# Kernel tuning notes

Measured on AMD Instinct MI355X. Metric: run time of the kernel, lower is better.

Reference implementation:

```python
import jax, jax.numpy as jnp
import numpy as np

BETA = 0.001  # commitment loss weight from __init__ default


def setup_inputs() -> dict:
    key = jax.random.key(0)
    k1, k2 = jax.random.split(key)
    N, INPUT_DIM = 8192, 1024
    S, K, D = 32, 1024, 32  # nsplits, num_embeddings, embedding_dim
    z = jax.random.normal(k1, (N, INPUT_DIM), dtype=jnp.float32)
    # Stacked codebook weights: one [K, D] embedding table per split.
    W = jax.random.normal(k2, (S, K, D), dtype=jnp.float32)
    return {"z": z, "W": W}


def reference(z, W):
    N, INPUT_DIM = z.shape
    S, K, D = W.shape
    zc = z.reshape(N, S, D)  # per-split chunks, matches torch.chunk(z, S, -1)
    # Squared euclidean distances ||z||^2 + ||w||^2 - 2 z.w  -> [N, S, K]
    d2 = (
        jnp.sum(zc * zc, axis=-1, keepdims=True)
        + jnp.sum(W * W, axis=-1)[None, :, :]
        - 2.0 * jnp.einsum("nsd,skd->nsk", zc, W)
    )
    idx = jnp.argmin(d2, axis=-1)  # [N, S]
    # Gather nearest codes: W[s, idx[n, s]] -> [N, S, D]
    zq = W[jnp.arange(S)[None, :], idx]
    # Sum over splits of per-split mse means; equal split sizes so this is
    # S * mean over the whole tensor.
    sg = jax.lax.stop_gradient
    loss = S * (
        jnp.mean((sg(zq) - zc) ** 2) + BETA * jnp.mean((zq - sg(zc)) ** 2)
    )
    # Straight-through estimator
    zq_st = zc + sg(zq - zc)
    return zq_st.reshape(N, INPUT_DIM), loss
```

## Files before the change

### kernel.cpp

```cpp
#include <hip/hip_runtime.h>
#include <math.h>

#define NN 8192
#define SS 32
#define DD 32
#define KK 1024
#define OUT_ELEMS ((size_t)NN * SS * DD)

#define LOSS_SCALE (32.0f * 1.001f / 8388608.0f)

typedef _Float16 half8 __attribute__((ext_vector_type(8)));
typedef float   floatx4 __attribute__((ext_vector_type(4)));

#define CH_TILES 4
#define CHUNK_K  (CH_TILES * 16)
#define NCHUNK   (KK / CHUNK_K)
#define RG 2
#define NBLOCKS ((NN / 128) * SS)


__global__ __launch_bounds__(256, 4) void vq_fused(const float* __restrict__ z,
                                                   const float* __restrict__ W,
                                                   float* __restrict__ out,
                                                   float* __restrict__ part) {
    __shared__ _Float16 bufH[2][CH_TILES][64][8];
    __shared__ _Float16 bufL[2][CH_TILES][64][8];
    __shared__ float    w2b[2][CHUNK_K];
    __shared__ int      lds_idx[4][32];
    __shared__ float    lds_part[4];

    const int s    = blockIdx.x & (SS - 1);
    const int n0b  = (blockIdx.x >> 5) * 128;
    const int tid  = threadIdx.x;
    const int wv   = tid >> 6;
    const int lane = tid & 63;
    const int col  = lane & 15;
    const int quad = lane >> 4;

    const float* __restrict__ Ws = W + (size_t)s * KK * DD;
    const int n0w = n0b + wv * 32;

    half8 zh[RG], zl[RG];
    #pragma unroll
    for (int rg = 0; rg < RG; ++rg) {
        const float* zp = z + (size_t)(n0w + rg * 16 + col) * (SS * DD) + s * DD + quad * 8;
        const float4 va = ((const float4*)zp)[0];
        const float4 vb = ((const float4*)zp)[1];
        const float src[8] = {va.x, va.y, va.z, va.w, vb.x, vb.y, vb.z, vb.w};
        #pragma unroll
        for (int j = 0; j < 8; ++j) {
            const float v = -2.0f * src[j];
            const _Float16 h = (_Float16)v;
            zh[rg][j] = h;
            zl[rg][j] = (_Float16)(v - (float)h);
        }
    }

    const float* __restrict__ stg = Ws + ((size_t)(wv * 16 + col)) * DD + quad * 8;

    floatx4 best[RG];
    int bi[RG][4];
    #pragma unroll
    for (int rg = 0; rg < RG; ++rg) {
        best[rg] = (floatx4){INFINITY, INFINITY, INFINITY, INFINITY};
        bi[rg][0] = bi[rg][1] = bi[rg][2] = bi[rg][3] = 0;
    }

    float4 pa = ((const float4*)stg)[0];
    float4 pb = ((const float4*)stg)[1];
    {
        const float src[8] = {pa.x, pa.y, pa.z, pa.w, pb.x, pb.y, pb.z, pb.w};
        half8 h8, l8; float ps = 0.0f;
        #pragma unroll
        for (int j = 0; j < 8; ++j) {
            const float v = src[j];
            ps = fmaf(v, v, ps);
            const _Float16 h = (_Float16)v;
            h8[j] = h;
            l8[j] = (_Float16)(v - (float)h);
        }
        ps += __shfl_xor(ps, 16, 64);
        ps += __shfl_xor(ps, 32, 64);
        *(half8*)&bufH[0][wv][lane][0] = h8;
        *(half8*)&bufL[0][wv][lane][0] = l8;
        if (quad == 0) w2b[0][wv * 16 + col] = ps;
    }
    __syncthreads();

    for (int c = 0; c < NCHUNK; ++c) {
        const int b = c & 1;
        if (c + 1 < NCHUNK) {
            const float* nsrc = stg + (size_t)(c + 1) * CHUNK_K * DD;
            pa = ((const float4*)nsrc)[0];
            pb = ((const float4*)nsrc)[1];
        }

        #pragma unroll
        for (int tt = 0; tt < CH_TILES; ++tt) {
            const half8 bh = *(const half8*)&bufH[b][tt][lane][0];
            const half8 bl = *(const half8*)&bufL[b][tt][lane][0];
            const float wv2 = w2b[b][tt * 16 + col];
            const floatx4 c0 = {wv2, wv2, wv2, wv2};
            const int tk = c * CH_TILES + tt;
            #pragma unroll
            for (int rg = 0; rg < RG; ++rg) {
                floatx4 acc = __builtin_amdgcn_mfma_f32_16x16x32_f16(zh[rg], bh, c0, 0, 0, 0);
                acc = __builtin_amdgcn_mfma_f32_16x16x32_f16(zl[rg], bh, acc, 0, 0, 0);
                acc = __builtin_amdgcn_mfma_f32_16x16x32_f16(zh[rg], bl, acc, 0, 0, 0);
                #pragma unroll
                for (int i = 0; i < 4; ++i) {
                    if (acc[i] < best[rg][i]) { best[rg][i] = acc[i]; bi[rg][i] = tk; }
                }
            }
        }

        if (c + 1 < NCHUNK) {
            const float src[8] = {pa.x, pa.y, pa.z, pa.w, pb.x, pb.y, pb.z, pb.w};
            half8 h8, l8; float ps = 0.0f;
            #pragma unroll
            for (int j = 0; j < 8; ++j) {
                const float v = src[j];
                ps = fmaf(v, v, ps);
                const _Float16 h = (_Float16)v;
                h8[j] = h;
                l8[j] = (_Float16)(v - (float)h);
            }
            ps += __shfl_xor(ps, 16, 64);
            ps += __shfl_xor(ps, 32, 64);
            const int nb = (c + 1) & 1;
            *(half8*)&bufH[nb][wv][lane][0] = h8;
            *(half8*)&bufL[nb][wv][lane][0] = l8;
            if (quad == 0) w2b[nb][wv * 16 + col] = ps;
            __syncthreads();
        }
    }

    #pragma unroll
    for (int rg = 0; rg < RG; ++rg) {
        #pragma unroll
        for (int i = 0; i < 4; ++i) {
            float v = best[rg][i];
            int   k = bi[rg][i] * 16 + col;
            #pragma unroll
            for (int m = 1; m < 16; m <<= 1) {
                const float vo = __shfl_xor(v, m, 64);
                const int   ko = __shfl_xor(k, m, 64);
                if (vo < v || (vo == v && ko < k)) { v = vo; k = ko; }
            }
            if (col == 0) lds_idx[wv][rg * 16 + quad * 4 + i] = k;
        }
    }
    __syncthreads();

    const int r  = lane & 31;
    const int dh = (lane >> 5) * 16;
    const int krow = lds_idx[wv][r];
    const float* wsrc = Ws + (size_t)krow * DD + dh;
    const size_t zoff = (size_t)(n0w + r) * (SS * DD) + s * DD + dh;
    const float* zsrc = z + zoff;
    float* od = out + zoff;
    float sq = 0.0f;
    #pragma unroll
    for (int cc = 0; cc < 4; ++cc) {
        const float4 wq = ((const float4*)wsrc)[cc];
        const float4 zv = ((const float4*)zsrc)[cc];
        const float d0 = wq.x - zv.x, d1 = wq.y - zv.y;
        const float d2 = wq.z - zv.z, d3 = wq.w - zv.w;
        sq = fmaf(d0, d0, sq); sq = fmaf(d1, d1, sq);
        sq = fmaf(d2, d2, sq); sq = fmaf(d3, d3, sq);
        ((float4*)od)[cc] = wq;
    }
    #pragma unroll
    for (int off = 32; off > 0; off >>= 1) sq += __shfl_down(sq, off, 64);

    if (lane == 0) lds_part[wv] = sq;
    __syncthreads();
    if (tid == 0)
        part[blockIdx.x] = lds_part[0] + lds_part[1] + lds_part[2] + lds_part[3];
}

__global__ __launch_bounds__(256) void vq_loss(const float* __restrict__ part,
                                               float* __restrict__ out) {
    __shared__ float l[4];
    const int tid = threadIdx.x;
    float sum = 0.0f;
    #pragma unroll
    for (int i = 0; i < NBLOCKS / 256; ++i) sum += part[tid + i * 256];
    #pragma unroll
    for (int off = 32; off > 0; off >>= 1) sum += __shfl_down(sum, off, 64);
    if ((tid & 63) == 0) l[tid >> 6] = sum;
    __syncthreads();
    if (tid == 0) out[OUT_ELEMS] = (l[0] + l[1] + l[2] + l[3]) * LOSS_SCALE;
}

extern "C" void kernel_launch(void* const* d_in, const int* in_sizes, int n_in,
                              void* d_out, int out_size, void* d_ws, size_t ws_size,
                              hipStream_t stream) {
    const float* z = (const float*)d_in[0];
    const float* W = (const float*)d_in[1];
    float* out  = (float*)d_out;
    float* part = (float*)d_ws;

    vq_fused<<<dim3(NBLOCKS), dim3(256), 0, stream>>>(z, W, out, part);
    vq_loss<<<dim3(1), dim3(256), 0, stream>>>(part, out);
}
```

Baseline: 152.5 us.

## Precompute split-fp16 codebook once in a prep kernel and stream fragments from global

Adds a prep kernel that converts W into hi/lo fp16 MFMA-ready fragments plus squared norms once per call. Before this, all 2048 blocks redid that conversion for their split. The main kernel now loads those fragments straight from global (L2) into registers with a two-tile register prefetch, and drops the LDS double buffer and its per-chunk __syncthreads. The cost is an extra kernel launch, extra workspace traffic, and more global-load latency that each wave must hide on its own.

```diff
diff --git a/kernel.cpp b/kernel.cpp
--- a/kernel.cpp
+++ b/kernel.cpp
@@ -12,22 +12,56 @@
 typedef _Float16 half8 __attribute__((ext_vector_type(8)));
 typedef float   floatx4 __attribute__((ext_vector_type(4)));
 
-#define CH_TILES 4
-#define CHUNK_K  (CH_TILES * 16)
-#define NCHUNK   (KK / CHUNK_K)
+#define TILES   (KK / 16)
 #define RG 2
 #define NBLOCKS ((NN / 128) * SS)
 
 
-__global__ __launch_bounds__(256, 4) void vq_fused(const float* __restrict__ z,
-                                                   const float* __restrict__ W,
-                                                   float* __restrict__ out,
-                                                   float* __restrict__ part) {
-    __shared__ _Float16 bufH[2][CH_TILES][64][8];
-    __shared__ _Float16 bufL[2][CH_TILES][64][8];
-    __shared__ float    w2b[2][CHUNK_K];
-    __shared__ int      lds_idx[4][32];
-    __shared__ float    lds_part[4];
+__global__ __launch_bounds__(256) void vq_prep(const float* __restrict__ W,
+                                               _Float16* __restrict__ wh,
+                                               _Float16* __restrict__ wl,
+                                               float* __restrict__ w2) {
+    const int g    = blockIdx.x * 256 + threadIdx.x;
+    const int l    = g & 63;
+    const int t    = (g >> 6) & 63;
+    const int s    = g >> 12;
+    const int col  = l & 15;
+    const int quad = l >> 4;
+    const int k    = t * 16 + col;
+
+    const float* src = W + ((size_t)s * KK + k) * DD + quad * 8;
+    const float4 a = ((const float4*)src)[0];
+    const float4 b = ((const float4*)src)[1];
+    const float v8[8] = {a.x, a.y, a.z, a.w, b.x, b.y, b.z, b.w};
+
+    float ps = 0.0f;
+    half8 h8, l8;
+    #pragma unroll
+    for (int j = 0; j < 8; ++j) {
+        const float v = v8[j];
+        ps = fmaf(v, v, ps);
+        const _Float16 h = (_Float16)v;
+        h8[j] = h;
+        l8[j] = (_Float16)(v - (float)h);
+    }
+    ps += __shfl_xor(ps, 16, 64);
+    ps += __shfl_xor(ps, 32, 64);
+    if (quad == 0) w2[(size_t)s * KK + k] = ps;
+
+    *(half8*)(wh + (size_t)g * 8) = h8;
+    *(half8*)(wl + (size_t)g * 8) = l8;
+}
+
+__global__ __launch_bounds__(256, 4) void vq_main(const float* __restrict__ z,
+                                                  const float* __restrict__ W,
+                                                  const _Float16* __restrict__ wh,
+                                                  const _Float16* __restrict__ wl,
+                                                  const float* __restrict__ w2,
+                                                  float* __restrict__ out,
+                                                  float* __restrict__ part) {
+    __shared__ float lds_w2[KK];
+    __shared__ int   lds_idx[4][32];
+    __shared__ float lds_part[4];
 
     const int s    = blockIdx.x & (SS - 1);
     const int n0b  = (blockIdx.x >> 5) * 128;
@@ -39,6 +73,11 @@
 
     const float* __restrict__ Ws = W + (size_t)s * KK * DD;
     const int n0w = n0b + wv * 32;
+
+    const float* w2s = w2 + (size_t)s * KK;
+    #pragma unroll
+    for (int j = 0; j < 4; ++j) lds_w2[tid + j * 256] = w2s[tid + j * 256];
+    __syncthreads();
 
     half8 zh[RG], zl[RG];
     #pragma unroll
@@ -56,7 +95,8 @@
         }
     }
 
-    const float* __restrict__ stg = Ws + ((size_t)(wv * 16 + col)) * DD + quad * 8;
+    const _Float16* __restrict__ bhp = wh + (size_t)s * (TILES * 64 * 8) + (size_t)lane * 8;
+    const _Float16* __restrict__ blp = wl + (size_t)s * (TILES * 64 * 8) + (size_t)lane * 8;
 
     floatx4 best[RG];
     int bi[RG][4];
@@ -66,42 +106,28 @@
         bi[rg][0] = bi[rg][1] = bi[rg][2] = bi[rg][3] = 0;
     }
 
-    float4 pa = ((const float4*)stg)[0];
-    float4 pb = ((const float4*)stg)[1];
-    {
-        const float src[8] = {pa.x, pa.y, pa.z, pa.w, pb.x, pb.y, pb.z, pb.w};
-        half8 h8, l8; float ps = 0.0f;
+    half8 bhA = *(const half8*)(bhp);
+    half8 blA = *(const half8*)(blp);
+    half8 bhB = *(const half8*)(bhp + 512);
+    half8 blB = *(const half8*)(blp + 512);
+
+    for (int t2 = 0; t2 < TILES / 2; ++t2) {
+        half8 nhA, nlA, nhB, nlB;
+        const bool more = (t2 + 1 < TILES / 2);
+        if (more) {
+            const size_t o = (size_t)(2 * t2 + 2) * 512;
+            nhA = *(const half8*)(bhp + o);
+            nlA = *(const half8*)(blp + o);
+            nhB = *(const half8*)(bhp + o + 512);
+            nlB = *(const half8*)(blp + o + 512);
+        }
         #pragma unroll
-        for (int j = 0; j < 8; ++j) {
-            const float v = src[j];
-            ps = fmaf(v, v, ps);
-            const _Float16 h = (_Float16)v;
-            h8[j] = h;
-            l8[j] = (_Float16)(v - (float)h);
-        }
-        ps += __shfl_xor(ps, 16, 64);
-        ps += __shfl_xor(ps, 32, 64);
-        *(half8*)&bufH[0][wv][lane][0] = h8;
-        *(half8*)&bufL[0][wv][lane][0] = l8;
-        if (quad == 0) w2b[0][wv * 16 + col] = ps;
-    }
-    __syncthreads();
-
-    for (int c = 0; c < NCHUNK; ++c) {
-        const int b = c & 1;
-        if (c + 1 < NCHUNK) {
-            const float* nsrc = stg + (size_t)(c + 1) * CHUNK_K * DD;
-            pa = ((const float4*)nsrc)[0];
-            pb = ((const float4*)nsrc)[1];
-        }
-
-        #pragma unroll
-        for (int tt = 0; tt < CH_TILES; ++tt) {
-            const half8 bh = *(const half8*)&bufH[b][tt][lane][0];
-            const half8 bl = *(const half8*)&bufL[b][tt][lane][0];
-            const float wv2 = w2b[b][tt * 16 + col];
+        for (int half = 0; half < 2; ++half) {
+            const int t = 2 * t2 + half;
+            const half8 bh = half ? bhB : bhA;
+            const half8 bl = half ? blB : blA;
+            const float wv2 = lds_w2[t * 16 + col];
             const floatx4 c0 = {wv2, wv2, wv2, wv2};
-            const int tk = c * CH_TILES + tt;
             #pragma unroll
             for (int rg = 0; rg < RG; ++rg) {
                 floatx4 acc = __builtin_amdgcn_mfma_f32_16x16x32_f16(zh[rg], bh, c0, 0, 0, 0);
@@ -109,30 +135,11 @@
                 acc = __builtin_amdgcn_mfma_f32_16x16x32_f16(zh[rg], bl, acc, 0, 0, 0);
                 #pragma unroll
                 for (int i = 0; i < 4; ++i) {
-                    if (acc[i] < best[rg][i]) { best[rg][i] = acc[i]; bi[rg][i] = tk; }
+                    if (acc[i] < best[rg][i]) { best[rg][i] = acc[i]; bi[rg][i] = t; }
                 }
             }
         }
-
-        if (c + 1 < NCHUNK) {
-            const float src[8] = {pa.x, pa.y, pa.z, pa.w, pb.x, pb.y, pb.z, pb.w};
-            half8 h8, l8; float ps = 0.0f;
-            #pragma unroll
-            for (int j = 0; j < 8; ++j) {
-                const float v = src[j];
-                ps = fmaf(v, v, ps);
-                const _Float16 h = (_Float16)v;
-                h8[j] = h;
-                l8[j] = (_Float16)(v - (float)h);
-            }
-            ps += __shfl_xor(ps, 16, 64);
-            ps += __shfl_xor(ps, 32, 64);
-            const int nb = (c + 1) & 1;
-            *(half8*)&bufH[nb][wv][lane][0] = h8;
-            *(half8*)&bufL[nb][wv][lane][0] = l8;
-            if (quad == 0) w2b[nb][wv * 16 + col] = ps;
-            __syncthreads();
-        }
+        if (more) { bhA = nhA; blA = nlA; bhB = nhB; blB = nlB; }
     }
 
     #pragma unroll
@@ -198,9 +205,14 @@
                               hipStream_t stream) {
     const float* z = (const float*)d_in[0];
     const float* W = (const float*)d_in[1];
-    float* out  = (float*)d_out;
-    float* part = (float*)d_ws;
-
-    vq_fused<<<dim3(NBLOCKS), dim3(256), 0, stream>>>(z, W, out, part);
+    float* out = (float*)d_out;
+
+    _Float16* wh = (_Float16*)d_ws;
+    _Float16* wl = wh + (size_t)SS * KK * DD;
+    float*    w2 = (float*)(wl + (size_t)SS * KK * DD);
+    float*    part = w2 + (size_t)SS * KK;
+
+    vq_prep<<<dim3((SS * KK * 4) / 256), dim3(256), 0, stream>>>(W, wh, wl, w2);
+    vq_main<<<dim3(NBLOCKS), dim3(256), 0, stream>>>(z, W, wh, wl, w2, out, part);
     vq_loss<<<dim3(1), dim3(256), 0, stream>>>(part, out);
 }
```

New measurement: 153.2 us. No clear change (+0.4%).
